# Performance work log

Measured on AMD Instinct MI355X. Metric: run time of the kernel, lower is better.

Reference implementation:

```python
import jax, jax.numpy as jnp
import numpy as np
import math

PI = math.pi
L = 6.0 * math.pi
EPS = 1e-5


def c19_activation(x, rho=4.0):
    scaled = x * (1.0 / PI)
    n = jnp.floor(scaled)
    t = scaled - n
    h = t * (1.0 - t)
    sgn = jnp.where(jnp.remainder(n, 2.0) < 1.0, 1.0, -1.0)
    core = PI * (sgn * h + rho * h * h)
    return jnp.where(x >= L, x - L, jnp.where(x <= -L, x + L, core))


def layer_norm(x, gamma, beta):
    mu = jnp.mean(x, axis=-1, keepdims=True)
    var = jnp.mean(jnp.square(x - mu), axis=-1, keepdims=True)
    return (x - mu) * jax.lax.rsqrt(var + EPS) * gamma + beta


def setup_inputs() -> dict:
    key = jax.random.key(0)
    ks = jax.random.split(key, 8)
    B, T, NB, D, DEPTH = 65536, 32, 8, 128, 4
    nl = DEPTH - 1  # 3 inner layers
    x = jax.random.normal(ks[0], (B, T, NB), dtype=jnp.float32)
    Wi = jax.random.normal(ks[1], (NB, D), dtype=jnp.float32) * 0.1   # input_proj (in, out)
    bi = jnp.zeros((D,), jnp.float32)
    Wo = jax.random.normal(ks[2], (D, NB), dtype=jnp.float32) * 0.1   # output_proj
    bo = jnp.zeros((NB,), jnp.float32)
    g_state = jnp.ones((D,), jnp.float32)
    b_state = jnp.zeros((D,), jnp.float32)
    Ws = jax.random.normal(ks[3], (nl, D, D), dtype=jnp.float32) * (1.0 / math.sqrt(D))
    bs = jnp.zeros((nl, D), jnp.float32)
    gs = jnp.ones((nl, D), jnp.float32)
    betas = jnp.zeros((nl, D), jnp.float32)
    return {"x": x, "Wi": Wi, "bi": bi, "Wo": Wo, "bo": bo,
            "g_state": g_state, "b_state": b_state,
            "Ws": Ws, "bs": bs, "gs": gs, "betas": betas}


def reference(x, Wi, bi, Wo, bo, g_state, b_state, Ws, bs, gs, betas):
    B, T, _ = x.shape
    D = Wi.shape[1]
    nl = Ws.shape[0]

    def step(h, xt):  # h: [B,D], xt: [B,NB]
        inp = xt @ Wi + bi
        state = 0.618 * layer_norm(h, g_state, b_state) + 0.382 * inp
        for i in range(nl):  # fixed small depth loop
            state = state + c19_activation(layer_norm(state, gs[i], betas[i]) @ Ws[i] + bs[i])
        out = state @ Wo + bo
        return state, out

    h0 = jnp.zeros((B, D), dtype=x.dtype)
    _, outs = jax.lax.scan(step, h0, jnp.swapaxes(x, 0, 1))  # outs: [T,B,NB]
    return jnp.swapaxes(outs, 0, 1)  # [B,T,NB]
```

## Files before the change

### kernel.cpp

```cpp
#include <hip/hip_runtime.h>
#include <math.h>

#define BDIM 1024
#define BR   64
#define D    128
#define SPD  130
#define WSP  130
#define SWOP 12
#define TT   32
#define NB   8
#define NL   3

typedef double v4d __attribute__((ext_vector_type(4)));

__device__ __forceinline__ double c19_act_d(double x) {
    const double PI_D = 3.14159265358979323846;
    const double L6   = 6.0 * PI_D;
    double scaled = x * (1.0 / PI_D);
    double n = floor(scaled);
    double t = scaled - n;
    double h = t * (1.0 - t);
    double halfn = n * 0.5;
    double fr = halfn - floor(halfn);
    double sgn = (fr < 0.25) ? 1.0 : -1.0;
    double core = PI_D * (sgn * h + 4.0 * h * h);
    double r = core;
    r = (x <= -L6) ? (x + L6) : r;
    r = (x >=  L6) ? (x - L6) : r;
    return r;
}

__global__ void miniphi_prep(const float* __restrict__ Ws, const float* __restrict__ gs,
                             double* __restrict__ wp) {
    int idx = blockIdx.x * 256 + threadIdx.x;
    wp[idx] = (double)gs[idx >> 7] * (double)Ws[idx];
}

__global__ __launch_bounds__(BDIM) void miniphi_kernel(
    const float* __restrict__ x,  const float* __restrict__ Wi, const float* __restrict__ bi,
    const float* __restrict__ Wo, const float* __restrict__ bo,
    const float* __restrict__ g_state, const float* __restrict__ b_state,
    const float* __restrict__ Ws, const float* __restrict__ bs,
    const float* __restrict__ gs, const float* __restrict__ betas,
    const double* __restrict__ wp,
    float* __restrict__ out)
{
    __shared__ double sState[BR][SPD];
    __shared__ double sWq[2][32][WSP];
    __shared__ float  sWi[NB][D];
    __shared__ float  sWo[D][SWOP];
    __shared__ float  sBi[D], sGst[D], sBst[D];
    __shared__ double sGsD[NL][D];
    __shared__ double sGW[NL][D];
    __shared__ double sBWbs[NL][D];
    __shared__ double sRstd[BR], sMu2[BR];
    __shared__ float  sBo[NB];
    __shared__ int    sPR[64][4], sPC[64][4];
    __shared__ int    sFlag;

    const int tid  = threadIdx.x;
    const int lane = tid & 63;
    const int wv   = tid >> 6;

    for (int i = tid; i < NB * D; i += BDIM) sWi[i >> 7][i & 127] = Wi[i];
    for (int i = tid; i < D * NB; i += BDIM) sWo[i >> 3][i & 7] = Wo[i];
    for (int i = tid; i < D; i += BDIM) { sBi[i] = bi[i]; sGst[i] = g_state[i]; sBst[i] = b_state[i]; }
    for (int i = tid; i < NL * D; i += BDIM) sGsD[i >> 7][i & 127] = (double)gs[i];
    if (tid < NB) sBo[tid] = bo[tid];
    for (int i = tid; i < BR * D; i += BDIM) sState[i >> 7][i & 127] = 0.0;
    if (tid < NL * D) {
        int ly = tid >> 7, c = tid & 127;
        const float* wl = Ws + (size_t)ly * D * D;
        double gw = 0.0, bw = 0.0;
        for (int k = 0; k < D; ++k) {
            double w = (double)wl[k * D + c];
            gw = fma((double)gs[ly * D + k], w, gw);
            bw = fma((double)betas[ly * D + k], w, bw);
        }
        sGW[ly][c] = gw;
        sBWbs[ly][c] = bw + (double)bs[ly * D + c];
    }

    if (wv == 0) {
        const int lm = lane & 15, lk = lane >> 4;
        v4d z = {0.0, 0.0, 0.0, 0.0};
        v4d p1 = __builtin_amdgcn_mfma_f64_16x16x4f64((double)lm, 1.0, z, 0, 0, 0);
        v4d p2 = __builtin_amdgcn_mfma_f64_16x16x4f64(1.0, (double)lm, z, 0, 0, 0);
        double pk = (double)(1 << lk);
        v4d p3 = __builtin_amdgcn_mfma_f64_16x16x4f64(pk, pk, z, 0, 0, 0);
        v4d p4 = __builtin_amdgcn_mfma_f64_16x16x4f64(1.0 + 0x1p-30, 1.0, z, 0, 0, 0);
        double pa5 = (lk == 0) ? 1.0 : 0x1p-52;
        v4d p5 = __builtin_amdgcn_mfma_f64_16x16x4f64(pa5, 1.0, z, 0, 0, 0);
        bool ok = true;
        #pragma unroll
        for (int i = 0; i < 4; ++i) {
            double v = p1[i]; int r = (int)(v * 0.25 + 0.5);
            ok = ok && (v == 4.0 * (double)r) && (r >= 0) && (r < 16);
            sPR[lane][i] = r;
            double w = p2[i]; int c2 = (int)(w * 0.25 + 0.5);
            ok = ok && (w == 4.0 * (double)c2) && (c2 >= 0) && (c2 < 16);
            sPC[lane][i] = c2;
            ok = ok && (p3[i] == 85.0);
            ok = ok && (p4[i] == 4.0 + 0x1p-28);
            ok = ok && (p5[i] == 1.0 + 3.0 * 0x1p-52);
        }
        unsigned long long bal = __ballot(ok ? 1 : 0);
        if (lane == 0) sFlag = (bal == 0xFFFFFFFFFFFFFFFFull) ? 1 : 0;
    }
    __syncthreads();

    const int useMfma = sFlag;
    int pr[4], pc[4];
    #pragma unroll
    for (int i = 0; i < 4; ++i) { pr[i] = sPR[lane][i]; pc[i] = sPC[lane][i]; }

    const int rLN = tid >> 4;
    const int sL  = tid & 15;
    const int lm  = lane & 15, lk = lane >> 4;
    const int rp  = wv >> 3;
    const int rb  = rp * 32;
    const int c0  = (wv & 7) * 16;
    const int r0v = wv * 4;
    const size_t rowg = (size_t)blockIdx.x * BR;

    #define STAGE_Q(LY, Q, QB)                                                      \
      { if (wp) {                                                                   \
          const double* src = wp + (((size_t)(LY) * D + (Q) * 32) * D);             \
          _Pragma("unroll")                                                         \
          for (int i_ = 0; i_ < 2; ++i_) {                                          \
              int kr_ = wv * 2 + i_;                                                \
              const double* g_ = src + (size_t)kr_ * D + lane * 2;                  \
              __builtin_amdgcn_global_load_lds(                                     \
                  (const __attribute__((address_space(1))) void*)g_,                \
                  (__attribute__((address_space(3))) void*)&sWq[QB][kr_][0],        \
                  16, 0, 0);                                                        \
          }                                                                         \
        } else {                                                                    \
          const float* src = Ws + (((size_t)(LY) * D + (Q) * 32) * D);              \
          const double* gl = &sGsD[LY][(Q) * 32];                                   \
          _Pragma("unroll")                                                         \
          for (int i_ = 0; i_ < 2; ++i_) {                                          \
              int kr_ = wv * 2 + i_;                                                \
              float2 w_ = *(const float2*)(src + (size_t)kr_ * D + lane * 2);       \
              double g_ = gl[kr_];                                                  \
              double2 o_; o_.x = g_ * (double)w_.x; o_.y = g_ * (double)w_.y;       \
              *(double2*)&sWq[QB][kr_][lane * 2] = o_;                              \
          }                                                                         \
        } }

    #define GEMM_Q(QB, QK)                                                          \
      if (useMfma) {                                                                \
          _Pragma("unroll")                                                         \
          for (int k0 = 0; k0 < 32; k0 += 4) {                                      \
              double b  = sWq[QB][k0 + lk][c0 + lm];                                \
              double a0 = sState[rb + lm     ][(QK) + k0 + lk];                     \
              double a1 = sState[rb + lm + 16][(QK) + k0 + lk];                     \
              acc0 = __builtin_amdgcn_mfma_f64_16x16x4f64(a0, b, acc0, 0, 0, 0);    \
              acc1 = __builtin_amdgcn_mfma_f64_16x16x4f64(a1, b, acc1, 0, 0, 0);    \
          }                                                                         \
      } else {                                                                      \
          _Pragma("unroll 4")                                                       \
          for (int kk = 0; kk < 32; kk += 2) {                                      \
              int kg = (QK) + kk;                                                   \
              double b00 = sWq[QB][kk][lane],     b01 = sWq[QB][kk][lane + 64];     \
              double b10 = sWq[QB][kk + 1][lane], b11 = sWq[QB][kk + 1][lane + 64]; \
              _Pragma("unroll")                                                     \
              for (int r = 0; r < 4; ++r) {                                         \
                  double2 a = *(const double2*)&sState[r0v + r][kg];                \
                  accv[r][0] = fma(a.y, b10, fma(a.x, b00, accv[r][0]));            \
                  accv[r][1] = fma(a.y, b11, fma(a.x, b01, accv[r][1]));            \
              }                                                                     \
          }                                                                         \
      }

    STAGE_Q(0, 0, 0)

    for (int t = 0; t < TT; ++t) {
        {
            const float* xp = x + (rowg + (size_t)rLN) * (TT * NB) + (size_t)t * NB;
            float4 xa = *(const float4*)(xp);
            float4 xb = *(const float4*)(xp + 4);
            double xv[8] = {(double)xa.x, (double)xa.y, (double)xa.z, (double)xa.w,
                            (double)xb.x, (double)xb.y, (double)xb.z, (double)xb.w};
            double v[8];
            #pragma unroll
            for (int j = 0; j < 8; ++j) v[j] = sState[rLN][sL + 16 * j];
            double sum = 0.0;
            #pragma unroll
            for (int j = 0; j < 8; ++j) sum += v[j];
            sum += __shfl_xor(sum, 1); sum += __shfl_xor(sum, 2);
            sum += __shfl_xor(sum, 4); sum += __shfl_xor(sum, 8);
            double mu = sum * (1.0 / 128.0);
            double sq = 0.0;
            #pragma unroll
            for (int j = 0; j < 8; ++j) { double dd = v[j] - mu; sq += dd * dd; }
            sq += __shfl_xor(sq, 1); sq += __shfl_xor(sq, 2);
            sq += __shfl_xor(sq, 4); sq += __shfl_xor(sq, 8);
            double rstd = 1.0 / sqrt(sq * (1.0 / 128.0) + 1e-5);
            #pragma unroll
            for (int j = 0; j < 8; ++j) {
                int c = sL + 16 * j;
                double inp = (double)sBi[c];
                #pragma unroll
                for (int k = 0; k < 8; ++k)
                    inp = fma(xv[k], (double)sWi[k][c], inp);
                double ln = (v[j] - mu) * rstd * (double)sGst[c] + (double)sBst[c];
                sState[rLN][c] = 0.618 * ln + 0.382 * inp;
            }
        }
        __syncthreads();

        for (int ly = 0; ly < NL; ++ly) {
            v4d acc0 = {0,0,0,0}, acc1 = {0,0,0,0};
            double accv[4][2];
            #pragma unroll
            for (int r = 0; r < 4; ++r) { accv[r][0] = 0.0; accv[r][1] = 0.0; }

            STAGE_Q(ly, 1, 1)
            GEMM_Q(0, 0)
            {
                double sum = 0.0;
                #pragma unroll
                for (int j = 0; j < 8; ++j) sum += sState[rLN][sL + 16 * j];
                sum += __shfl_xor(sum, 1); sum += __shfl_xor(sum, 2);
                sum += __shfl_xor(sum, 4); sum += __shfl_xor(sum, 8);
                double mu = sum * (1.0 / 128.0);
                double sq = 0.0;
                #pragma unroll
                for (int j = 0; j < 8; ++j) { double dd = sState[rLN][sL + 16 * j] - mu; sq += dd * dd; }
                sq += __shfl_xor(sq, 1); sq += __shfl_xor(sq, 2);
                sq += __shfl_xor(sq, 4); sq += __shfl_xor(sq, 8);
                double rstd = 1.0 / sqrt(sq * (1.0 / 128.0) + 1e-5);
                if (sL == 0) { sRstd[rLN] = rstd; sMu2[rLN] = mu * rstd; }
            }
            __syncthreads();

            STAGE_Q(ly, 2, 0)
            GEMM_Q(1, 32)
            __syncthreads();

            STAGE_Q(ly, 3, 1)
            GEMM_Q(0, 64)
            __syncthreads();

            if (ly + 1 < NL) { STAGE_Q(ly + 1, 0, 0) } else { STAGE_Q(0, 0, 0) }
            GEMM_Q(1, 96)
            __syncthreads();

            if (useMfma) {
                #pragma unroll
                for (int i = 0; i < 4; ++i) {
                    int col = c0 + pc[i];
                    double gwc = sGW[ly][col], bwc = sBWbs[ly][col];
                    int R0 = rb + pr[i];
                    double y0 = fma(sRstd[R0],      acc0[i], fma(-sMu2[R0],      gwc, bwc));
                    double y1 = fma(sRstd[R0 + 16], acc1[i], fma(-sMu2[R0 + 16], gwc, bwc));
                    sState[R0][col]      += c19_act_d(y0);
                    sState[R0 + 16][col] += c19_act_d(y1);
                }
            } else {
                double gwc0 = sGW[ly][lane],   gwc1 = sGW[ly][lane + 64];
                double bwc0 = sBWbs[ly][lane], bwc1 = sBWbs[ly][lane + 64];
                #pragma unroll
                for (int r = 0; r < 4; ++r) {
                    int R = r0v + r;
                    double rs = sRstd[R], m2 = sMu2[R];
                    double y0 = fma(rs, accv[r][0], fma(-m2, gwc0, bwc0));
                    double y1 = fma(rs, accv[r][1], fma(-m2, gwc1, bwc1));
                    sState[R][lane]      += c19_act_d(y0);
                    sState[R][lane + 64] += c19_act_d(y1);
                }
            }
            __syncthreads();
        }

        {
            double accj[8];
            #pragma unroll
            for (int j = 0; j < 8; ++j) accj[j] = 0.0;
            #pragma unroll
            for (int u = 0; u < 8; ++u) {
                int k = sL + 16 * u;
                double s = sState[rLN][k];
                float4 w0 = *(const float4*)&sWo[k][0];
                float4 w1 = *(const float4*)&sWo[k][4];
                accj[0] = fma(s, (double)w0.x, accj[0]);
                accj[1] = fma(s, (double)w0.y, accj[1]);
                accj[2] = fma(s, (double)w0.z, accj[2]);
                accj[3] = fma(s, (double)w0.w, accj[3]);
                accj[4] = fma(s, (double)w1.x, accj[4]);
                accj[5] = fma(s, (double)w1.y, accj[5]);
                accj[6] = fma(s, (double)w1.z, accj[6]);
                accj[7] = fma(s, (double)w1.w, accj[7]);
            }
            #pragma unroll
            for (int j = 0; j < 8; ++j) {
                accj[j] += __shfl_xor(accj[j], 1);
                accj[j] += __shfl_xor(accj[j], 2);
                accj[j] += __shfl_xor(accj[j], 4);
                accj[j] += __shfl_xor(accj[j], 8);
            }
            double o = accj[0];
            #pragma unroll
            for (int j = 1; j < 8; ++j) o = (sL == j) ? accj[j] : o;
            if (sL < NB)
                out[((rowg + (size_t)rLN) * TT + (size_t)t) * NB + sL] =
                    (float)(o + (double)sBo[sL]);
        }
    }
    #undef GEMM_Q
    #undef STAGE_Q
}

extern "C" void kernel_launch(void* const* d_in, const int* in_sizes, int n_in,
                              void* d_out, int out_size, void* d_ws, size_t ws_size,
                              hipStream_t stream) {
    const float* x       = (const float*)d_in[0];
    const float* Wi      = (const float*)d_in[1];
    const float* bi      = (const float*)d_in[2];
    const float* Wo      = (const float*)d_in[3];
    const float* bo      = (const float*)d_in[4];
    const float* g_state = (const float*)d_in[5];
    const float* b_state = (const float*)d_in[6];
    const float* Ws      = (const float*)d_in[7];
    const float* bs      = (const float*)d_in[8];
    const float* gs      = (const float*)d_in[9];
    const float* betas   = (const float*)d_in[10];
    float* out = (float*)d_out;

    const size_t wp_bytes = (size_t)NL * D * D * sizeof(double);
    double* wp = (ws_size >= wp_bytes) ? (double*)d_ws : nullptr;
    if (wp) {
        dim3 pgrid(NL * D * D / 256), pblock(256);
        hipLaunchKernelGGL(miniphi_prep, pgrid, pblock, 0, stream, Ws, gs, wp);
    }

    const int B = in_sizes[0] / (TT * NB);
    dim3 grid(B / BR), block(BDIM);
    hipLaunchKernelGGL(miniphi_kernel, grid, block, 0, stream,
                       x, Wi, bi, Wo, bo, g_state, b_state, Ws, bs, gs, betas, wp, out);
}
```

Before: 5.146 ms.

## Halve block size and shrink shared memory to raise occupancy

Blocks drop from 1024 threads and 64 rows to 512 threads and 32 rows. The weight staging buffer shrinks to 16-row eighths, so each layer now runs eight stage/GEMM steps instead of four. Small shared copies of Wi, Wo, the biases and gains are removed and read straight from global memory, and the MFMA permutation probe now runs in every wave with results kept in registers. This cuts LDS per block so more blocks fit per CU, at the cost of twice as many barriers per layer and more global or cache reads in the inner loops.

```diff
diff --git a/kernel.cpp b/kernel.cpp
--- a/kernel.cpp
+++ b/kernel.cpp
@@ -1,12 +1,11 @@
 #include <hip/hip_runtime.h>
 #include <math.h>
 
-#define BDIM 1024
-#define BR   64
+#define BDIM 512
+#define BR   32
 #define D    128
 #define SPD  130
 #define WSP  130
-#define SWOP 12
 #define TT   32
 #define NB   8
 #define NL   3
@@ -46,28 +45,18 @@
     float* __restrict__ out)
 {
     __shared__ double sState[BR][SPD];
-    __shared__ double sWq[2][32][WSP];
-    __shared__ float  sWi[NB][D];
-    __shared__ float  sWo[D][SWOP];
-    __shared__ float  sBi[D], sGst[D], sBst[D];
-    __shared__ double sGsD[NL][D];
+    __shared__ double sWq[2][16][WSP];
     __shared__ double sGW[NL][D];
     __shared__ double sBWbs[NL][D];
     __shared__ double sRstd[BR], sMu2[BR];
-    __shared__ float  sBo[NB];
-    __shared__ int    sPR[64][4], sPC[64][4];
     __shared__ int    sFlag;
 
     const int tid  = threadIdx.x;
     const int lane = tid & 63;
     const int wv   = tid >> 6;
 
-    for (int i = tid; i < NB * D; i += BDIM) sWi[i >> 7][i & 127] = Wi[i];
-    for (int i = tid; i < D * NB; i += BDIM) sWo[i >> 3][i & 7] = Wo[i];
-    for (int i = tid; i < D; i += BDIM) { sBi[i] = bi[i]; sGst[i] = g_state[i]; sBst[i] = b_state[i]; }
-    for (int i = tid; i < NL * D; i += BDIM) sGsD[i >> 7][i & 127] = (double)gs[i];
-    if (tid < NB) sBo[tid] = bo[tid];
     for (int i = tid; i < BR * D; i += BDIM) sState[i >> 7][i & 127] = 0.0;
+    if (tid == 0) sFlag = 1;
     if (tid < NL * D) {
         int ly = tid >> 7, c = tid & 127;
         const float* wl = Ws + (size_t)ly * D * D;
@@ -80,9 +69,11 @@
         sGW[ly][c] = gw;
         sBWbs[ly][c] = bw + (double)bs[ly * D + c];
     }
-
-    if (wv == 0) {
-        const int lm = lane & 15, lk = lane >> 4;
+    __syncthreads();
+
+    const int lm = lane & 15, lk = lane >> 4;
+    int pr[4], pc[4];
+    {
         v4d z = {0.0, 0.0, 0.0, 0.0};
         v4d p1 = __builtin_amdgcn_mfma_f64_16x16x4f64((double)lm, 1.0, z, 0, 0, 0);
         v4d p2 = __builtin_amdgcn_mfma_f64_16x16x4f64(1.0, (double)lm, z, 0, 0, 0);
@@ -96,36 +87,29 @@
         for (int i = 0; i < 4; ++i) {
             double v = p1[i]; int r = (int)(v * 0.25 + 0.5);
             ok = ok && (v == 4.0 * (double)r) && (r >= 0) && (r < 16);
-            sPR[lane][i] = r;
+            pr[i] = r;
             double w = p2[i]; int c2 = (int)(w * 0.25 + 0.5);
             ok = ok && (w == 4.0 * (double)c2) && (c2 >= 0) && (c2 < 16);
-            sPC[lane][i] = c2;
+            pc[i] = c2;
             ok = ok && (p3[i] == 85.0);
             ok = ok && (p4[i] == 4.0 + 0x1p-28);
             ok = ok && (p5[i] == 1.0 + 3.0 * 0x1p-52);
         }
         unsigned long long bal = __ballot(ok ? 1 : 0);
-        if (lane == 0) sFlag = (bal == 0xFFFFFFFFFFFFFFFFull) ? 1 : 0;
+        if (lane == 0 && bal != 0xFFFFFFFFFFFFFFFFull) atomicAnd(&sFlag, 0);
     }
     __syncthreads();
-
     const int useMfma = sFlag;
-    int pr[4], pc[4];
-    #pragma unroll
-    for (int i = 0; i < 4; ++i) { pr[i] = sPR[lane][i]; pc[i] = sPC[lane][i]; }
 
     const int rLN = tid >> 4;
     const int sL  = tid & 15;
-    const int lm  = lane & 15, lk = lane >> 4;
-    const int rp  = wv >> 3;
-    const int rb  = rp * 32;
-    const int c0  = (wv & 7) * 16;
+    const int c0  = wv * 16;
     const int r0v = wv * 4;
     const size_t rowg = (size_t)blockIdx.x * BR;
 
-    #define STAGE_Q(LY, Q, QB)                                                      \
+    #define STAGE_E(LY, E, QB)                                                      \
       { if (wp) {                                                                   \
-          const double* src = wp + (((size_t)(LY) * D + (Q) * 32) * D);             \
+          const double* src = wp + (((size_t)(LY) * D + (E) * 16) * D);             \
           _Pragma("unroll")                                                         \
           for (int i_ = 0; i_ < 2; ++i_) {                                          \
               int kr_ = wv * 2 + i_;                                                \
@@ -136,32 +120,32 @@
                   16, 0, 0);                                                        \
           }                                                                         \
         } else {                                                                    \
-          const float* src = Ws + (((size_t)(LY) * D + (Q) * 32) * D);              \
-          const double* gl = &sGsD[LY][(Q) * 32];                                   \
+          const float* src = Ws + (((size_t)(LY) * D + (E) * 16) * D);              \
+          const float* gl  = gs + (LY) * D + (E) * 16;                              \
           _Pragma("unroll")                                                         \
           for (int i_ = 0; i_ < 2; ++i_) {                                          \
               int kr_ = wv * 2 + i_;                                                \
               float2 w_ = *(const float2*)(src + (size_t)kr_ * D + lane * 2);       \
-              double g_ = gl[kr_];                                                  \
+              double g_ = (double)gl[kr_];                                          \
               double2 o_; o_.x = g_ * (double)w_.x; o_.y = g_ * (double)w_.y;       \
               *(double2*)&sWq[QB][kr_][lane * 2] = o_;                              \
           }                                                                         \
         } }
 
-    #define GEMM_Q(QB, QK)                                                          \
+    #define GEMM_E(QB, KB)                                                          \
       if (useMfma) {                                                                \
           _Pragma("unroll")                                                         \
-          for (int k0 = 0; k0 < 32; k0 += 4) {                                      \
+          for (int k0 = 0; k0 < 16; k0 += 4) {                                      \
               double b  = sWq[QB][k0 + lk][c0 + lm];                                \
-              double a0 = sState[rb + lm     ][(QK) + k0 + lk];                     \
-              double a1 = sState[rb + lm + 16][(QK) + k0 + lk];                     \
+              double a0 = sState[lm     ][(KB) + k0 + lk];                          \
+              double a1 = sState[lm + 16][(KB) + k0 + lk];                          \
               acc0 = __builtin_amdgcn_mfma_f64_16x16x4f64(a0, b, acc0, 0, 0, 0);    \
               acc1 = __builtin_amdgcn_mfma_f64_16x16x4f64(a1, b, acc1, 0, 0, 0);    \
           }                                                                         \
       } else {                                                                      \
-          _Pragma("unroll 4")                                                       \
-          for (int kk = 0; kk < 32; kk += 2) {                                      \
-              int kg = (QK) + kk;                                                   \
+          _Pragma("unroll")                                                         \
+          for (int kk = 0; kk < 16; kk += 2) {                                      \
+              int kg = (KB) + kk;                                                   \
               double b00 = sWq[QB][kk][lane],     b01 = sWq[QB][kk][lane + 64];     \
               double b10 = sWq[QB][kk + 1][lane], b11 = sWq[QB][kk + 1][lane + 64]; \
               _Pragma("unroll")                                                     \
@@ -173,7 +157,7 @@
           }                                                                         \
       }
 
-    STAGE_Q(0, 0, 0)
+    STAGE_E(0, 0, 0)
 
     for (int t = 0; t < TT; ++t) {
         {
@@ -200,11 +184,11 @@
             #pragma unroll
             for (int j = 0; j < 8; ++j) {
                 int c = sL + 16 * j;
-                double inp = (double)sBi[c];
+                double inp = (double)bi[c];
                 #pragma unroll
                 for (int k = 0; k < 8; ++k)
-                    inp = fma(xv[k], (double)sWi[k][c], inp);
-                double ln = (v[j] - mu) * rstd * (double)sGst[c] + (double)sBst[c];
+                    inp = fma(xv[k], (double)Wi[k * D + c], inp);
+                double ln = (v[j] - mu) * rstd * (double)g_state[c] + (double)b_state[c];
                 sState[rLN][c] = 0.618 * ln + 0.382 * inp;
             }
         }
@@ -216,8 +200,8 @@
             #pragma unroll
             for (int r = 0; r < 4; ++r) { accv[r][0] = 0.0; accv[r][1] = 0.0; }
 
-            STAGE_Q(ly, 1, 1)
-            GEMM_Q(0, 0)
+            STAGE_E(ly, 1, 1)
+            GEMM_E(0, 0)
             {
                 double sum = 0.0;
                 #pragma unroll
@@ -235,16 +219,14 @@
             }
             __syncthreads();
 
-            STAGE_Q(ly, 2, 0)
-            GEMM_Q(1, 32)
-            __syncthreads();
-
-            STAGE_Q(ly, 3, 1)
-            GEMM_Q(0, 64)
-            __syncthreads();
-
-            if (ly + 1 < NL) { STAGE_Q(ly + 1, 0, 0) } else { STAGE_Q(0, 0, 0) }
-            GEMM_Q(1, 96)
+            STAGE_E(ly, 2, 0) GEMM_E(1, 16)  __syncthreads();
+            STAGE_E(ly, 3, 1) GEMM_E(0, 32)  __syncthreads();
+            STAGE_E(ly, 4, 0) GEMM_E(1, 48)  __syncthreads();
+            STAGE_E(ly, 5, 1) GEMM_E(0, 64)  __syncthreads();
+            STAGE_E(ly, 6, 0) GEMM_E(1, 80)  __syncthreads();
+            STAGE_E(ly, 7, 1) GEMM_E(0, 96)  __syncthreads();
+            if (ly + 1 < NL) { STAGE_E(ly + 1, 0, 0) } else { STAGE_E(0, 0, 0) }
+            GEMM_E(1, 112)
             __syncthreads();
 
             if (useMfma) {
@@ -252,7 +234,7 @@
                 for (int i = 0; i < 4; ++i) {
                     int col = c0 + pc[i];
                     double gwc = sGW[ly][col], bwc = sBWbs[ly][col];
-                    int R0 = rb + pr[i];
+                    int R0 = pr[i];
                     double y0 = fma(sRstd[R0],      acc0[i], fma(-sMu2[R0],      gwc, bwc));
                     double y1 = fma(sRstd[R0 + 16], acc1[i], fma(-sMu2[R0 + 16], gwc, bwc));
                     sState[R0][col]      += c19_act_d(y0);
@@ -282,8 +264,8 @@
             for (int u = 0; u < 8; ++u) {
                 int k = sL + 16 * u;
                 double s = sState[rLN][k];
-                float4 w0 = *(const float4*)&sWo[k][0];
-                float4 w1 = *(const float4*)&sWo[k][4];
+                float4 w0 = *(const float4*)&Wo[k * NB];
+                float4 w1 = *(const float4*)&Wo[k * NB + 4];
                 accj[0] = fma(s, (double)w0.x, accj[0]);
                 accj[1] = fma(s, (double)w0.y, accj[1]);
                 accj[2] = fma(s, (double)w0.z, accj[2]);
@@ -305,11 +287,11 @@
             for (int j = 1; j < 8; ++j) o = (sL == j) ? accj[j] : o;
             if (sL < NB)
                 out[((rowg + (size_t)rLN) * TT + (size_t)t) * NB + sL] =
-                    (float)(o + (double)sBo[sL]);
+                    (float)(o + (double)bo[sL]);
         }
     }
-    #undef GEMM_Q
-    #undef STAGE_Q
+    #undef GEMM_E
+    #undef STAGE_E
 }
 
 extern "C" void kernel_launch(void* const* d_in, const int* in_sizes, int n_in,
```

After: 14.23 ms. 177% more time.
